# Kernel tuning notes

Measured on AMD Instinct MI355X. Metric: run time of the kernel, lower is better.

## Reference

```python
import jax, jax.numpy as jnp
import numpy as np

DIM = 768
HEADS = 12
HEAD_DIM = DIM // HEADS
WS = 32                      # window_size (Wh == Ww)
N = WS * WS + 1              # tokens = patches + CLS
B = 8
NUM_REL = (2 * WS - 1) * (2 * WS - 1) + 3


def _rel_pos_index():
    # Mirrors the torch buffer construction (meshgrid indexing='ij').
    coords = np.stack(np.meshgrid(np.arange(WS), np.arange(WS), indexing='ij')).reshape(2, -1)
    rel = (coords[:, :, None] - coords[:, None, :]).transpose(1, 2, 0)  # [M, M, 2]
    rel[..., 0] += WS - 1
    rel[..., 1] += WS - 1
    rel[..., 0] *= 2 * WS - 1
    idx = np.zeros((N, N), dtype=np.int32)
    idx[1:, 1:] = rel.sum(-1)
    idx[0, :] = NUM_REL - 3
    idx[:, 0] = NUM_REL - 2
    idx[0, 0] = NUM_REL - 1
    return idx


def setup_inputs() -> dict:
    key = jax.random.key(0)
    ks = jax.random.split(key, 4)
    s = DIM ** -0.5
    return {
        "x": jax.random.normal(ks[0], (B, N, DIM), dtype=jnp.float32),
        "qkv_w": jax.random.normal(ks[1], (3 * DIM, DIM), dtype=jnp.float32) * s,
        "q_bias": jnp.zeros((DIM,), dtype=jnp.float32),
        "v_bias": jnp.zeros((DIM,), dtype=jnp.float32),
        "rpb_table": jax.random.normal(ks[2], (NUM_REL, HEADS), dtype=jnp.float32) * 0.02,
        "proj_w": jax.random.normal(ks[3], (DIM, DIM), dtype=jnp.float32) * s,
        "proj_b": jnp.zeros((DIM,), dtype=jnp.float32),
        "rel_pos_index": jnp.asarray(_rel_pos_index()),
    }


def reference(x, qkv_w, q_bias, v_bias, rpb_table, proj_w, proj_b, rel_pos_index):
    Bx, Nx, C = x.shape
    scale = HEAD_DIM ** -0.5
    # qkv bias = [q_bias, zeros, v_bias] (k has no bias)
    qkv_bias = jnp.concatenate([q_bias, jnp.zeros_like(v_bias), v_bias])
    qkv = x @ qkv_w.T + qkv_bias                           # [B, N, 3*C]
    qkv = qkv.reshape(Bx, Nx, 3, HEADS, HEAD_DIM).transpose(2, 0, 3, 1, 4)
    q, k, v = qkv[0] * scale, qkv[1], qkv[2]               # [B, H, N, d]
    attn = jnp.einsum('bhqd,bhkd->bhqk', q, k)             # [B, H, N, N]
    rpb = rpb_table[rel_pos_index]                         # [N, N, H] gather
    attn = attn + rpb.transpose(2, 0, 1)[None]             # broadcast over batch
    attn = jax.nn.softmax(attn, axis=-1)
    out = jnp.einsum('bhqk,bhkd->bhqd', attn, v)           # [B, H, N, d]
    out = out.transpose(0, 2, 1, 3).reshape(Bx, Nx, -1)    # [B, N, C]
    return out @ proj_w.T + proj_b
```

## Files before the change

### kernel.cpp

```cpp
#include <hip/hip_runtime.h>

typedef _Float16 f16;
typedef __attribute__((ext_vector_type(4))) _Float16 f16x4;
typedef __attribute__((ext_vector_type(8))) _Float16 f16x8;
typedef __attribute__((ext_vector_type(4))) float f32x4;

#define BATCH 8
#define NTOK 1025
#define DIM 768
#define HEADS 12
#define HD 64
#define MTOT (BATCH * NTOK)
#define MPAD 8320
#define NQP2 1152
#define NKP 1088
#define NUMREL 3972

#define DMA_FENCE asm volatile("s_waitcnt vmcnt(0)" ::: "memory")

__device__ __forceinline__ int imin(int a, int b) { return a < b ? a : b; }

__device__ __forceinline__ void gl_lds16(const f16* g, f16* l) {
  __builtin_amdgcn_global_load_lds(
      (const __attribute__((address_space(1))) unsigned int*)g,
      (__attribute__((address_space(3))) unsigned int*)l, 16, 0, 0);
}

__global__ __launch_bounds__(256) void cast3(const float* __restrict__ s0,
                                             f16* __restrict__ d0, int n0,
                                             const float* __restrict__ s1,
                                             f16* __restrict__ d1, int n1,
                                             const float* __restrict__ s2,
                                             f16* __restrict__ d2, int n2) {
  const float* s = (blockIdx.y == 0) ? s0 : (blockIdx.y == 1) ? s1 : s2;
  f16* d = (blockIdx.y == 0) ? d0 : (blockIdx.y == 1) ? d1 : d2;
  int n = (blockIdx.y == 0) ? n0 : (blockIdx.y == 1) ? n1 : n2;
  for (size_t i = ((size_t)blockIdx.x * 256 + threadIdx.x) * 8; i < (size_t)n;
       i += (size_t)gridDim.x * 256 * 8) {
    float4 a = *(const float4*)(s + i);
    float4 b = *(const float4*)(s + i + 4);
    f16x8 r;
    r[0] = (f16)a.x; r[1] = (f16)a.y; r[2] = (f16)a.z; r[3] = (f16)a.w;
    r[4] = (f16)b.x; r[5] = (f16)b.y; r[6] = (f16)b.z; r[7] = (f16)b.w;
    *(f16x8*)(d + i) = r;
  }
}

__global__ __launch_bounds__(256) void rpb_t(const float* __restrict__ rpb,
                                             float* __restrict__ rpbt) {
  int i = blockIdx.x * 256 + threadIdx.x;
  if (i >= NUMREL * HEADS) return;
  int idx = i / HEADS, h = i - idx * HEADS;
  rpbt[(size_t)h * NUMREL + idx] = rpb[i];
}

__global__ __launch_bounds__(512) void qkv_gemm(
    const f16* __restrict__ Ah, const f16* __restrict__ Bh,
    const float* __restrict__ q_bias, const float* __restrict__ v_bias,
    f16* __restrict__ qb, f16* __restrict__ kb, f16* __restrict__ vtb) {
  __shared__ f16 As[128][64];
  __shared__ f16 Bs[256][64];
  const int tid = threadIdx.x;
  const int lane = tid & 63, w = tid >> 6;
  const int wm = w >> 2, wn = w & 3;
  const int lr = lane & 15, lg = lane >> 4;
  const int tN = blockIdx.x;
  const int tM = blockIdx.y;
  const int r8 = lane >> 3;
  const int swch = (lane & 7) ^ r8;
  const int lr7 = lr & 7;

  const f16* Ab = Ah + ((size_t)tM * 128 + r8) * DIM + swch * 8;
  const f16* Bb = Bh + ((size_t)tN * 256 + r8) * DIM + swch * 8;

  f32x4 acc[4][4] = {};

  for (int kt = 0; kt < 12; kt++) {
#pragma unroll
    for (int pp = 0; pp < 2; pp++) {
      int rowb = w * 16 + pp * 8;
      gl_lds16(Ab + (size_t)rowb * DIM + kt * 64, &As[rowb][0]);
    }
#pragma unroll
    for (int pp = 0; pp < 4; pp++) {
      int rowb = w * 32 + pp * 8;
      gl_lds16(Bb + (size_t)rowb * DIM + kt * 64, &Bs[rowb][0]);
    }
    DMA_FENCE;
    __syncthreads();
#pragma unroll
    for (int ks = 0; ks < 2; ks++) {
      f16x8 af[4], bf[4];
      int rc = ((ks * 4 + lg) ^ lr7) * 8;
#pragma unroll
      for (int i = 0; i < 4; i++) {
        af[i] = *(const f16x8*)(&As[wm * 64 + i * 16 + lr][rc]);
        bf[i] = *(const f16x8*)(&Bs[wn * 64 + i * 16 + lr][rc]);
      }
#pragma unroll
      for (int mi = 0; mi < 4; mi++)
#pragma unroll
        for (int ni = 0; ni < 4; ni++)
          acc[mi][ni] = __builtin_amdgcn_mfma_f32_16x16x32_f16(
              af[mi], bf[ni], acc[mi][ni], 0, 0, 0);
    }
    __syncthreads();
  }

  const int which = tN / 3;
  const int nb = tN % 3;
#pragma unroll
  for (int mi = 0; mi < 4; mi++) {
#pragma unroll
    for (int ni = 0; ni < 4; ni++) {
      int ncol = nb * 256 + wn * 64 + ni * 16 + lr;
      int h = ncol >> 6, dd = ncol & 63;
      float bias = 0.f;
      if (which == 0) bias = q_bias[ncol];
      if (which == 2) bias = v_bias[ncol];
#pragma unroll
      for (int r = 0; r < 4; r++) {
        int m = tM * 128 + wm * 64 + mi * 16 + lg * 4 + r;
        if (m >= MTOT) continue;
        int b = m / NTOK;
        int t = m - b * NTOK;
        int bh = b * HEADS + h;
        float v = acc[mi][ni][r] + bias;
        if (which == 0)
          qb[((size_t)bh * NQP2 + t) * HD + dd] = (f16)(v * 0.125f);
        else if (which == 1)
          kb[((size_t)bh * NKP + t) * HD + dd] = (f16)v;
        else
          vtb[((size_t)bh * HD + dd) * NKP + t] = (f16)v;
      }
    }
  }
}

__global__ __launch_bounds__(512) void attn_kernel(
    const f16* __restrict__ qb, const f16* __restrict__ kb,
    const f16* __restrict__ vtb, const float* __restrict__ rpbt,
    f16* __restrict__ ob) {
  __shared__ f16 Ks[2][64][64];
  __shared__ f16 Vs[2][64][64];
  __shared__ f16 Plds[8][16][72];
  const int tid = threadIdx.x;
  const int lane = tid & 63, w = tid >> 6;
  const int lr = lane & 15, lg = lane >> 4;
  const int b = blockIdx.x & 7;
  const int t5 = blockIdx.x >> 3;
  const int qpair = t5 % 5;
  const int h = t5 / 5;
  const int qblk = qpair * 2 + (w >> 2);
  const int bh = b * HEADS + h;
  const int q0 = qblk * 128 + (w & 3) * 32;

  const f16* kbase = kb + (size_t)bh * NKP * HD;
  const f16* vbase = vtb + (size_t)bh * HD * NKP;

  const int srow8 = lane >> 3;
  const int swch = (lane & 7) ^ srow8;

  {
    int row = w * 8 + srow8;
    gl_lds16(kbase + (size_t)row * HD + swch * 8, &Ks[0][w * 8][0]);
    gl_lds16(vbase + (size_t)row * NKP + swch * 8, &Vs[0][w * 8][0]);
  }

  f16x8 aq[2][2];
#pragma unroll
  for (int g = 0; g < 2; g++) {
    const f16* qp = qb + ((size_t)bh * NQP2 + q0 + g * 16 + lr) * HD + lg * 8;
    aq[g][0] = *(const f16x8*)(qp);
    aq[g][1] = *(const f16x8*)(qp + 32);
  }

  int qd0[2], qm0[2], qz[2];
#pragma unroll
  for (int g = 0; g < 2; g++) {
    int q = imin(q0 + g * 16 + lr, 1024);
    qz[g] = (q == 0);
    int qq = (q > 0 ? q : 1) - 1;
    qd0[g] = qq >> 5;
    qm0[g] = qq & 31;
  }
  const float* rph = rpbt + (size_t)h * NUMREL;

  float lsum[2] = {0.f, 0.f};
  f32x4 oacc[2][4] = {};
  const int sw8 = lr & 7;

  for (int kt = 0; kt < 17; kt++) {
    const int bi = kt & 1;
    DMA_FENCE;
    __syncthreads();
    if (kt + 1 < 17) {
      int row = w * 8 + srow8;
      gl_lds16(kbase + (size_t)((kt + 1) * 64 + row) * HD + swch * 8,
               &Ks[bi ^ 1][w * 8][0]);
      gl_lds16(vbase + (size_t)row * NKP + (kt + 1) * 64 + swch * 8,
               &Vs[bi ^ 1][w * 8][0]);
    }
    f32x4 s[2][4];
#pragma unroll
    for (int c = 0; c < 4; c++)
#pragma unroll
      for (int r = 0; r < 4; r++) {
        int kv = kt * 64 + c * 16 + lg * 4 + r;
        int kk = kv - 1;
        int kd = kk >> 5, km = kk & 31;
#pragma unroll
        for (int g = 0; g < 2; g++) {
          int idx = (qd0[g] - kd + 31) * 63 + (qm0[g] - km + 31);
          idx = qz[g] ? (NUMREL - 3) : idx;
          if (kv == 0) idx = qz[g] ? (NUMREL - 1) : (NUMREL - 2);
          idx = (kv >= NTOK) ? 0 : idx;
          float bv = rph[idx];
          s[g][c][r] = (kv >= NTOK) ? -30000.f : bv;
        }
      }
#pragma unroll
    for (int c = 0; c < 4; c++) {
      f16x8 kf0 = *(const f16x8*)(&Ks[bi][c * 16 + lr][(lg ^ sw8) * 8]);
      f16x8 kf1 = *(const f16x8*)(&Ks[bi][c * 16 + lr][((lg + 4) ^ sw8) * 8]);
      s[0][c] = __builtin_amdgcn_mfma_f32_16x16x32_f16(kf0, aq[0][0], s[0][c], 0, 0, 0);
      s[0][c] = __builtin_amdgcn_mfma_f32_16x16x32_f16(kf1, aq[0][1], s[0][c], 0, 0, 0);
      s[1][c] = __builtin_amdgcn_mfma_f32_16x16x32_f16(kf0, aq[1][0], s[1][c], 0, 0, 0);
      s[1][c] = __builtin_amdgcn_mfma_f32_16x16x32_f16(kf1, aq[1][1], s[1][c], 0, 0, 0);
    }
#pragma unroll
    for (int g = 0; g < 2; g++)
#pragma unroll
      for (int c = 0; c < 4; c++)
#pragma unroll
        for (int r = 0; r < 4; r++) {
          float p = __expf(s[g][c][r]);
          s[g][c][r] = p;
          lsum[g] += p;
        }
    f16x8 ap[2][2];
#pragma unroll
    for (int g = 0; g < 2; g++) {
#pragma unroll
      for (int c = 0; c < 4; c++) {
        f16x4 pk;
        pk[0] = (f16)s[g][c][0];
        pk[1] = (f16)s[g][c][1];
        pk[2] = (f16)s[g][c][2];
        pk[3] = (f16)s[g][c][3];
        *(f16x4*)(&Plds[w][lr][c * 16 + lg * 4]) = pk;
      }
      ap[g][0] = *(const f16x8*)(&Plds[w][lr][lg * 8]);
      ap[g][1] = *(const f16x8*)(&Plds[w][lr][32 + lg * 8]);
    }
#pragma unroll
    for (int dblk = 0; dblk < 4; dblk++) {
      f16x8 vf0 = *(const f16x8*)(&Vs[bi][dblk * 16 + lr][(lg ^ sw8) * 8]);
      f16x8 vf1 = *(const f16x8*)(&Vs[bi][dblk * 16 + lr][((lg + 4) ^ sw8) * 8]);
      oacc[0][dblk] = __builtin_amdgcn_mfma_f32_16x16x32_f16(ap[0][0], vf0, oacc[0][dblk], 0, 0, 0);
      oacc[0][dblk] = __builtin_amdgcn_mfma_f32_16x16x32_f16(ap[0][1], vf1, oacc[0][dblk], 0, 0, 0);
      oacc[1][dblk] = __builtin_amdgcn_mfma_f32_16x16x32_f16(ap[1][0], vf0, oacc[1][dblk], 0, 0, 0);
      oacc[1][dblk] = __builtin_amdgcn_mfma_f32_16x16x32_f16(ap[1][1], vf1, oacc[1][dblk], 0, 0, 0);
    }
  }
#pragma unroll
  for (int g = 0; g < 2; g++) {
    float ls = lsum[g];
    ls += __shfl_xor(ls, 16);
    ls += __shfl_xor(ls, 32);
    float inv[4];
#pragma unroll
    for (int r = 0; r < 4; r++) inv[r] = 1.f / __shfl(ls, lg * 4 + r);
#pragma unroll
    for (int dblk = 0; dblk < 4; dblk++)
#pragma unroll
      for (int r = 0; r < 4; r++) {
        int qg = q0 + g * 16 + lg * 4 + r;
        if (qg >= NTOK) continue;
        float v = oacc[g][dblk][r] * inv[r];
        ob[((size_t)(b * NTOK + qg)) * DIM + h * HD + dblk * 16 + lr] = (f16)v;
      }
  }
}

__global__ __launch_bounds__(512) void proj_gemm(const f16* __restrict__ Ah,
                                                 const f16* __restrict__ Bh,
                                                 const float* __restrict__ pb,
                                                 float* __restrict__ out) {
  __shared__ f16 As[128][64];
  __shared__ f16 Bs[256][64];
  const int tid = threadIdx.x;
  const int lane = tid & 63, w = tid >> 6;
  const int wm = w >> 2, wn = w & 3;
  const int lr = lane & 15, lg = lane >> 4;
  const int tN = blockIdx.x;
  const int tM = blockIdx.y;
  const int r8 = lane >> 3;
  const int swch = (lane & 7) ^ r8;
  const int lr7 = lr & 7;

  const f16* Ab = Ah + ((size_t)tM * 128 + r8) * DIM + swch * 8;
  const f16* Bb = Bh + ((size_t)tN * 256 + r8) * DIM + swch * 8;

  f32x4 acc[4][4] = {};

  for (int kt = 0; kt < 12; kt++) {
#pragma unroll
    for (int pp = 0; pp < 2; pp++) {
      int rowb = w * 16 + pp * 8;
      gl_lds16(Ab + (size_t)rowb * DIM + kt * 64, &As[rowb][0]);
    }
#pragma unroll
    for (int pp = 0; pp < 4; pp++) {
      int rowb = w * 32 + pp * 8;
      gl_lds16(Bb + (size_t)rowb * DIM + kt * 64, &Bs[rowb][0]);
    }
    DMA_FENCE;
    __syncthreads();
#pragma unroll
    for (int ks = 0; ks < 2; ks++) {
      f16x8 af[4], bf[4];
      int rc = ((ks * 4 + lg) ^ lr7) * 8;
#pragma unroll
      for (int i = 0; i < 4; i++) {
        af[i] = *(const f16x8*)(&As[wm * 64 + i * 16 + lr][rc]);
        bf[i] = *(const f16x8*)(&Bs[wn * 64 + i * 16 + lr][rc]);
      }
#pragma unroll
      for (int mi = 0; mi < 4; mi++)
#pragma unroll
        for (int ni = 0; ni < 4; ni++)
          acc[mi][ni] = __builtin_amdgcn_mfma_f32_16x16x32_f16(
              af[mi], bf[ni], acc[mi][ni], 0, 0, 0);
    }
    __syncthreads();
  }

#pragma unroll
  for (int mi = 0; mi < 4; mi++) {
#pragma unroll
    for (int ni = 0; ni < 4; ni++) {
      int n = tN * 256 + wn * 64 + ni * 16 + lr;
      float bias = pb[n];
#pragma unroll
      for (int r = 0; r < 4; r++) {
        int m = tM * 128 + wm * 64 + mi * 16 + lg * 4 + r;
        if (m >= MTOT) continue;
        out[(size_t)m * DIM + n] = acc[mi][ni][r] + bias;
      }
    }
  }
}

extern "C" void kernel_launch(void* const* d_in, const int* in_sizes, int n_in,
                              void* d_out, int out_size, void* d_ws,
                              size_t ws_size, hipStream_t stream) {
  const float* x = (const float*)d_in[0];
  const float* qkv_w = (const float*)d_in[1];
  const float* q_bias = (const float*)d_in[2];
  const float* v_bias = (const float*)d_in[3];
  const float* rpb = (const float*)d_in[4];
  const float* proj_w = (const float*)d_in[5];
  const float* proj_b = (const float*)d_in[6];
  float* out = (float*)d_out;

  f16* xh = (f16*)d_ws;
  f16* wh = xh + (size_t)MPAD * DIM;
  f16* pwh = wh + (size_t)3 * DIM * DIM;
  f16* qb = pwh + (size_t)DIM * DIM;
  f16* kb = qb + (size_t)BATCH * HEADS * NQP2 * HD;
  f16* vtb = kb + (size_t)BATCH * HEADS * NKP * HD;
  f16* ob = vtb + (size_t)BATCH * HEADS * NKP * HD;
  float* rpbt = (float*)(ob + (size_t)MPAD * DIM);

  cast3<<<dim3(1024, 3), 256, 0, stream>>>(
      x, xh, MTOT * DIM, qkv_w, wh, 3 * DIM * DIM, proj_w, pwh, DIM * DIM);
  rpb_t<<<dim3(187), 256, 0, stream>>>(rpb, rpbt);
  qkv_gemm<<<dim3(9, 65), 512, 0, stream>>>(xh, wh, q_bias, v_bias, qb, kb,
                                            vtb);
  attn_kernel<<<dim3(BATCH * 5 * HEADS), 512, 0, stream>>>(qb, kb, vtb, rpbt,
                                                           ob);
  proj_gemm<<<dim3(3, 65), 512, 0, stream>>>(ob, pwh, proj_b, out);
}
```

Baseline: 280.3 us.

## Stage K/V through registers and prefetch relative-position bias one tile ahead

Replaces the double-buffered global_load_lds DMA path with register-staged K/V loads that are written into a single LDS buffer, fetched two tiles ahead. The relative-position-bias gather for the next key tile is issued after the QK MFMAs and kept in fp16 registers, so its latency overlaps compute. The bias index is also simplified by precomputing a per-query base. In exchange this adds two barriers per iteration, uses more registers, and rounds the bias to fp16.

Result: no change. 278.1 us (-0.8%).

```diff
diff --git a/kernel.cpp b/kernel.cpp
--- a/kernel.cpp
+++ b/kernel.cpp
@@ -141,8 +141,8 @@
     const f16* __restrict__ qb, const f16* __restrict__ kb,
     const f16* __restrict__ vtb, const float* __restrict__ rpbt,
     f16* __restrict__ ob) {
-  __shared__ f16 Ks[2][64][64];
-  __shared__ f16 Vs[2][64][64];
+  __shared__ f16 Ks[64][64];
+  __shared__ f16 Vs[64][64];
   __shared__ f16 Plds[8][16][72];
   const int tid = threadIdx.x;
   const int lane = tid & 63, w = tid >> 6;
@@ -160,12 +160,10 @@
 
   const int srow8 = lane >> 3;
   const int swch = (lane & 7) ^ srow8;
-
-  {
-    int row = w * 8 + srow8;
-    gl_lds16(kbase + (size_t)row * HD + swch * 8, &Ks[0][w * 8][0]);
-    gl_lds16(vbase + (size_t)row * NKP + swch * 8, &Vs[0][w * 8][0]);
-  }
+  const int row = w * 8 + srow8;
+
+  f16x8 rk = *(const f16x8*)(kbase + (size_t)row * HD + swch * 8);
+  f16x8 rv = *(const f16x8*)(vbase + (size_t)row * NKP + swch * 8);
 
   f16x8 aq[2][2];
 #pragma unroll
@@ -175,59 +173,70 @@
     aq[g][1] = *(const f16x8*)(qp + 32);
   }
 
-  int qd0[2], qm0[2], qz[2];
+  int qz[2], qbase[2];
 #pragma unroll
   for (int g = 0; g < 2; g++) {
     int q = imin(q0 + g * 16 + lr, 1024);
     qz[g] = (q == 0);
     int qq = (q > 0 ? q : 1) - 1;
-    qd0[g] = qq >> 5;
-    qm0[g] = qq & 31;
+    qbase[g] = ((qq >> 5) + 31) * 63 + (qq & 31) + 31;
   }
   const float* rph = rpbt + (size_t)h * NUMREL;
+
+#define FETCH_BIAS(KT, DST)                                                   \
+  {                                                                           \
+    _Pragma("unroll") for (int g = 0; g < 2; g++) {                           \
+      f16 vals[16];                                                           \
+      _Pragma("unroll") for (int c = 0; c < 4; c++)                           \
+          _Pragma("unroll") for (int r = 0; r < 4; r++) {                     \
+        int kv = (KT) * 64 + c * 16 + lg * 4 + r;                             \
+        int kk = kv - 1;                                                      \
+        int t = (kk >> 5) * 63 + (kk & 31);                                   \
+        int idx = qbase[g] - t;                                               \
+        idx = qz[g] ? (NUMREL - 3) : idx;                                     \
+        if (kv == 0) idx = qz[g] ? (NUMREL - 1) : (NUMREL - 2);               \
+        idx = (kv >= NTOK) ? 0 : idx;                                         \
+        float bv = rph[idx];                                                  \
+        vals[c * 4 + r] = (f16)((kv >= NTOK) ? -30000.f : bv);                \
+      }                                                                       \
+      DST[g][0] = *(const f16x8*)(&vals[0]);                                  \
+      DST[g][1] = *(const f16x8*)(&vals[8]);                                  \
+    }                                                                         \
+  }
+
+  f16x8 bb[2][2], nb[2][2];
+  FETCH_BIAS(0, bb);
+
+  *(f16x8*)(&Ks[w * 8][0] + lane * 8) = rk;
+  *(f16x8*)(&Vs[w * 8][0] + lane * 8) = rv;
+  __syncthreads();
+  rk = *(const f16x8*)(kbase + (size_t)(64 + row) * HD + swch * 8);
+  rv = *(const f16x8*)(vbase + (size_t)row * NKP + 64 + swch * 8);
 
   float lsum[2] = {0.f, 0.f};
   f32x4 oacc[2][4] = {};
   const int sw8 = lr & 7;
 
   for (int kt = 0; kt < 17; kt++) {
-    const int bi = kt & 1;
-    DMA_FENCE;
-    __syncthreads();
-    if (kt + 1 < 17) {
-      int row = w * 8 + srow8;
-      gl_lds16(kbase + (size_t)((kt + 1) * 64 + row) * HD + swch * 8,
-               &Ks[bi ^ 1][w * 8][0]);
-      gl_lds16(vbase + (size_t)row * NKP + (kt + 1) * 64 + swch * 8,
-               &Vs[bi ^ 1][w * 8][0]);
-    }
     f32x4 s[2][4];
 #pragma unroll
-    for (int c = 0; c < 4; c++)
-#pragma unroll
-      for (int r = 0; r < 4; r++) {
-        int kv = kt * 64 + c * 16 + lg * 4 + r;
-        int kk = kv - 1;
-        int kd = kk >> 5, km = kk & 31;
-#pragma unroll
-        for (int g = 0; g < 2; g++) {
-          int idx = (qd0[g] - kd + 31) * 63 + (qm0[g] - km + 31);
-          idx = qz[g] ? (NUMREL - 3) : idx;
-          if (kv == 0) idx = qz[g] ? (NUMREL - 1) : (NUMREL - 2);
-          idx = (kv >= NTOK) ? 0 : idx;
-          float bv = rph[idx];
-          s[g][c][r] = (kv >= NTOK) ? -30000.f : bv;
-        }
+    for (int g = 0; g < 2; g++)
+#pragma unroll
+      for (int c = 0; c < 4; c++) {
+        const f16* src = (const f16*)&bb[g][c >> 1];
+#pragma unroll
+        for (int r = 0; r < 4; r++) s[g][c][r] = (float)src[(c & 1) * 4 + r];
       }
 #pragma unroll
     for (int c = 0; c < 4; c++) {
-      f16x8 kf0 = *(const f16x8*)(&Ks[bi][c * 16 + lr][(lg ^ sw8) * 8]);
-      f16x8 kf1 = *(const f16x8*)(&Ks[bi][c * 16 + lr][((lg + 4) ^ sw8) * 8]);
+      f16x8 kf0 = *(const f16x8*)(&Ks[c * 16 + lr][(lg ^ sw8) * 8]);
+      f16x8 kf1 = *(const f16x8*)(&Ks[c * 16 + lr][((lg + 4) ^ sw8) * 8]);
       s[0][c] = __builtin_amdgcn_mfma_f32_16x16x32_f16(kf0, aq[0][0], s[0][c], 0, 0, 0);
       s[0][c] = __builtin_amdgcn_mfma_f32_16x16x32_f16(kf1, aq[0][1], s[0][c], 0, 0, 0);
       s[1][c] = __builtin_amdgcn_mfma_f32_16x16x32_f16(kf0, aq[1][0], s[1][c], 0, 0, 0);
       s[1][c] = __builtin_amdgcn_mfma_f32_16x16x32_f16(kf1, aq[1][1], s[1][c], 0, 0, 0);
     }
+    if (kt + 1 < 17) FETCH_BIAS(kt + 1, nb);
 #pragma unroll
     for (int g = 0; g < 2; g++)
 #pragma unroll
@@ -255,12 +264,27 @@
     }
 #pragma unroll
     for (int dblk = 0; dblk < 4; dblk++) {
-      f16x8 vf0 = *(const f16x8*)(&Vs[bi][dblk * 16 + lr][(lg ^ sw8) * 8]);
-      f16x8 vf1 = *(const f16x8*)(&Vs[bi][dblk * 16 + lr][((lg + 4) ^ sw8) * 8]);
+      f16x8 vf0 = *(const f16x8*)(&Vs[dblk * 16 + lr][(lg ^ sw8) * 8]);
+      f16x8 vf1 = *(const f16x8*)(&Vs[dblk * 16 + lr][((lg + 4) ^ sw8) * 8]);
       oacc[0][dblk] = __builtin_amdgcn_mfma_f32_16x16x32_f16(ap[0][0], vf0, oacc[0][dblk], 0, 0, 0);
       oacc[0][dblk] = __builtin_amdgcn_mfma_f32_16x16x32_f16(ap[0][1], vf1, oacc[0][dblk], 0, 0, 0);
       oacc[1][dblk] = __builtin_amdgcn_mfma_f32_16x16x32_f16(ap[1][0], vf0, oacc[1][dblk], 0, 0, 0);
       oacc[1][dblk] = __builtin_amdgcn_mfma_f32_16x16x32_f16(ap[1][1], vf1, oacc[1][dblk], 0, 0, 0);
+    }
+    if (kt + 1 < 17) {
+      __syncthreads();
+      *(f16x8*)(&Ks[w * 8][0] + lane * 8) = rk;
+      *(f16x8*)(&Vs[w * 8][0] + lane * 8) = rv;
+      __syncthreads();
+      if (kt + 2 < 17) {
+        rk = *(const f16x8*)(kbase + (size_t)((kt + 2) * 64 + row) * HD + swch * 8);
+        rv = *(const f16x8*)(vbase + (size_t)row * NKP + (kt + 2) * 64 + swch * 8);
+      }
+    }
+#pragma unroll
+    for (int g = 0; g < 2; g++) {
+      bb[g][0] = nb[g][0];
+      bb[g][1] = nb[g][1];
     }
   }
 #pragma unroll
```
